# Performance work log

Hardware: AMD Instinct MI355X
Metric: run time of the kernel (lower is better)

The kernel has to match this reference:

```python
import jax, jax.numpy as jnp
import numpy as np
import math

D_MODEL = 1024
NUM_HEADS = 16
B, S = 2, 2048


def setup_inputs() -> dict:
    key = jax.random.key(0)
    ks = jax.random.split(key, 12)
    s = 0.02
    inp = {
        "q": jax.random.normal(ks[0], (B, S, D_MODEL), jnp.float32),
        "k": jax.random.normal(ks[1], (B, S, D_MODEL), jnp.float32),
        "v": jax.random.normal(ks[2], (B, S, D_MODEL), jnp.float32),
        "W_q": jax.random.normal(ks[3], (D_MODEL, D_MODEL), jnp.float32) * s,
        "b_q": jnp.zeros((D_MODEL,), jnp.float32),
        "W_k": jax.random.normal(ks[4], (D_MODEL, D_MODEL), jnp.float32) * s,
        "b_k": jnp.zeros((D_MODEL,), jnp.float32),
        "W_v": jax.random.normal(ks[5], (D_MODEL, D_MODEL), jnp.float32) * s,
        "b_v": jnp.zeros((D_MODEL,), jnp.float32),
        "W_o": jax.random.normal(ks[6], (D_MODEL, D_MODEL), jnp.float32) * s,
        "b_o": jnp.zeros((D_MODEL,), jnp.float32),
        # broadcastable causal mask [1,1,S,S]; masked positions are 0
        "mask": jnp.tril(jnp.ones((S, S), jnp.int32))[None, None, :, :],
    }
    return inp


def reference(q, k, v, W_q, b_q, W_k, b_k, W_v, b_v, W_o, b_o, mask):
    H, d_k = NUM_HEADS, D_MODEL // NUM_HEADS
    Bq, Sq, D = q.shape
    Sk = k.shape[1]
    # Linear projections (torch Linear: x @ W.T + b), split heads -> [B,H,S,d_k]
    qh = (q @ W_q.T + b_q).reshape(Bq, Sq, H, d_k).transpose(0, 2, 1, 3)
    kh = (k @ W_k.T + b_k).reshape(Bq, Sk, H, d_k).transpose(0, 2, 1, 3)
    vh = (v @ W_v.T + b_v).reshape(Bq, Sk, H, d_k).transpose(0, 2, 1, 3)
    # scores [B,H,Sq,Sk]
    scores = jnp.einsum("bhqd,bhkd->bhqk", qh, kh) / math.sqrt(d_k)
    scores = jnp.where(mask == 0, jnp.float32(-jnp.inf), scores)
    attn = jax.nn.softmax(scores, axis=-1)
    context = jnp.einsum("bhqk,bhkd->bhqd", attn, vh)
    context = context.transpose(0, 2, 1, 3).reshape(Bq, Sq, D)
    return context @ W_o.T + b_o
```

## Files before the change

### kernel.cpp

```cpp
#include <hip/hip_runtime.h>
#include <hip/hip_bf16.h>

using f32x4  = __attribute__((ext_vector_type(4))) float;
using f32x16 = __attribute__((ext_vector_type(16))) float;
using short8 = __attribute__((ext_vector_type(8))) short;
using us8    = __attribute__((ext_vector_type(8))) unsigned short;
using us4    = __attribute__((ext_vector_type(4))) unsigned short;
using fl4    = __attribute__((ext_vector_type(4))) float;

__device__ __forceinline__ unsigned short f2bf(float f){
    unsigned u = __builtin_bit_cast(unsigned, f);
    u += 0x7FFF + ((u >> 16) & 1);
    return (unsigned short)(u >> 16);
}

__device__ __forceinline__ unsigned cvtpk_bf16(float lo, float hi){
    unsigned r;
    asm volatile("v_cvt_pk_bf16_f32 %0, %1, %2" : "=v"(r) : "v"(lo), "v"(hi));
    return r;
}

__device__ __forceinline__ void pl32swap(unsigned &a, unsigned &b){
    asm volatile("v_permlane32_swap_b32 %0, %1" : "+v"(a), "+v"(b));
}

__device__ __forceinline__ void gload16(const unsigned short* g, unsigned short* l) {
    __builtin_amdgcn_global_load_lds(
        (const __attribute__((address_space(1))) unsigned int*)g,
        (__attribute__((address_space(3))) unsigned int*)l, 16, 0, 0);
}

__global__ __launch_bounds__(256)
void conv_bf16(const float* __restrict__ s0, const float* __restrict__ s1, const float* __restrict__ s2,
               const float* __restrict__ s3, const float* __restrict__ s4, const float* __restrict__ s5,
               const float* __restrict__ s6,
               unsigned short* __restrict__ d0, unsigned short* __restrict__ d1, unsigned short* __restrict__ d2,
               unsigned short* __restrict__ d3, unsigned short* __restrict__ d4, unsigned short* __restrict__ d5,
               unsigned short* __restrict__ d6,
               int nbig4, int nsml4)
{
    const int z = blockIdx.z;
    const float* s = (z==0)?s0:(z==1)?s1:(z==2)?s2:(z==3)?s3:(z==4)?s4:(z==5)?s5:s6;
    unsigned short* d = (z==0)?d0:(z==1)?d1:(z==2)?d2:(z==3)?d3:(z==4)?d4:(z==5)?d5:d6;
    const int n4 = (z < 3) ? nbig4 : nsml4;
    const int stride = gridDim.x * blockDim.x;
    for (int i = blockIdx.x * blockDim.x + threadIdx.x; i < n4; i += stride) {
        fl4 v = ((const fl4*)s)[i];
        us4 o = { f2bf(v[0]), f2bf(v[1]), f2bf(v[2]), f2bf(v[3]) };
        ((us4*)d)[i] = o;
    }
}

template<bool OBF16>
__global__ __launch_bounds__(256, 2)
void gemm_bf16(const unsigned short* __restrict__ A0, const unsigned short* __restrict__ A1,
               const unsigned short* __restrict__ A2,
               const unsigned short* __restrict__ W0, const unsigned short* __restrict__ W1,
               const unsigned short* __restrict__ W2,
               const float* __restrict__ B0, const float* __restrict__ B1, const float* __restrict__ B2,
               void* __restrict__ O0, void* __restrict__ O1, void* __restrict__ O2,
               int M, int N, int K)
{
    const int z = blockIdx.z;
    const unsigned short* Ap = (z==0)?A0:(z==1)?A1:A2;
    const unsigned short* Wp = (z==0)?W0:(z==1)?W1:W2;
    const float* bp = (z==0)?B0:(z==1)?B1:B2;
    void* Op = (z==0)?O0:(z==1)?O1:O2;

    const int tid = threadIdx.x, lane = tid & 63, w = tid >> 6;
    const int wr = w >> 1, wc = w & 1;
    const int l15 = lane & 15, l4 = lane >> 4;
    const int bm = blockIdx.y, bn = blockIdx.x;

    __shared__ unsigned short As[2][128 * 64];
    __shared__ unsigned short Bs[2][128 * 64];

    f32x4 acc[4][4];
    #pragma unroll
    for (int i = 0; i < 4; i++)
        #pragma unroll
        for (int j = 0; j < 4; j++) acc[i][j] = (f32x4){0.f, 0.f, 0.f, 0.f};

    const int KT = K >> 6;
    const int srow = lane >> 3;
    const int scol = (lane & 7) * 8;

    auto stage = [&](int buf, int kt) {
        #pragma unroll
        for (int i = 0; i < 4; i++) {
            const int chunk = w * 4 + i;
            const int row = chunk * 8 + srow;
            gload16(Ap + (size_t)(bm * 128 + row) * K + kt * 64 + scol, &As[buf][chunk * 512]);
            gload16(Wp + (size_t)(bn * 128 + row) * K + kt * 64 + scol, &Bs[buf][chunk * 512]);
        }
    };

    stage(0, 0);
    int cur = 0;
    for (int kt = 0; kt < KT; ++kt) {
        if (kt + 1 < KT) {
            stage(cur ^ 1, kt + 1);
            asm volatile("s_waitcnt vmcnt(8)" ::: "memory");
        } else {
            asm volatile("s_waitcnt vmcnt(0)" ::: "memory");
        }
        __builtin_amdgcn_s_barrier();

        short8 af[4][2], bfr[4][2];
        #pragma unroll
        for (int mf = 0; mf < 4; mf++)
            #pragma unroll
            for (int kf = 0; kf < 2; kf++)
                af[mf][kf] = *(const short8*)&As[cur][(wr * 64 + mf * 16 + l15) * 64 + kf * 32 + l4 * 8];
        #pragma unroll
        for (int nf = 0; nf < 4; nf++)
            #pragma unroll
            for (int kf = 0; kf < 2; kf++)
                bfr[nf][kf] = *(const short8*)&Bs[cur][(wc * 64 + nf * 16 + l15) * 64 + kf * 32 + l4 * 8];
        #pragma unroll
        for (int mf = 0; mf < 4; mf++)
            #pragma unroll
            for (int nf = 0; nf < 4; nf++)
                #pragma unroll
                for (int kf = 0; kf < 2; kf++)
                    acc[mf][nf] = __builtin_amdgcn_mfma_f32_16x16x32_bf16(af[mf][kf], bfr[nf][kf], acc[mf][nf], 0, 0, 0);

        __builtin_amdgcn_s_barrier();
        cur ^= 1;
    }

    #pragma unroll
    for (int mf = 0; mf < 4; mf++) {
        int row = bm * 128 + wr * 64 + mf * 16 + l4 * 4;
        #pragma unroll
        for (int nf = 0; nf < 4; nf++) {
            int col = bn * 128 + wc * 64 + nf * 16 + l15;
            float bv = bp[col];
            #pragma unroll
            for (int r = 0; r < 4; r++) {
                float vv = acc[mf][nf][r] + bv;
                if constexpr (OBF16)
                    ((unsigned short*)Op)[(size_t)(row + r) * N + col] = f2bf(vv);
                else
                    ((float*)Op)[(size_t)(row + r) * N + col] = vv;
            }
        }
    }
}

__global__ __launch_bounds__(256)
void transpose_v(const unsigned short* __restrict__ Vp, unsigned short* __restrict__ VpT)
{
    const int bh = blockIdx.y, b = bh >> 4, h = bh & 15;
    const int s0 = blockIdx.x * 64;
    const int tid = threadIdx.x;
    __shared__ unsigned short T[64 * 64];
    #pragma unroll
    for (int i = 0; i < 2; i++) {
        int cc = i * 256 + tid, r = cc >> 3, c = cc & 7;
        us8 v = *(const us8*)(Vp + (size_t)(b * 2048 + s0 + r) * 1024 + h * 64 + c * 8);
        int off = (r * 128 + c * 16) ^ ((((r & 7) ^ ((r >> 3) & 7))) << 4);
        *(us8*)((char*)T + off) = v;
    }
    __syncthreads();
    #pragma unroll
    for (int i = 0; i < 2; i++) {
        int cc = i * 256 + tid, d = cc >> 3, c = cc & 7;
        us8 o;
        #pragma unroll
        for (int j = 0; j < 8; j++) {
            int s = c * 8 + j;
            int off = (s * 128 + d * 2) ^ ((((s & 7) ^ ((s >> 3) & 7))) << 4);
            o[j] = *(const unsigned short*)((const char*)T + off);
        }
        *(us8*)(VpT + ((size_t)bh * 64 + d) * 2048 + s0 + c * 8) = o;
    }
}

__global__ __launch_bounds__(128)
void attn_causal(const unsigned short* __restrict__ Qp,
                 const unsigned short* __restrict__ Kp,
                 const unsigned short* __restrict__ VpT,
                 unsigned short* __restrict__ Ctx)
{
    const int S = 2048, D = 1024;
    const int bh = blockIdx.y, b = bh >> 4, h = bh & 15;
    const int pairIdx = blockIdx.x;
    const int tid = threadIdx.x, w = tid >> 6, lane = tid & 63;
    const int l31 = lane & 31, hi = lane >> 5;

    __shared__ unsigned short Ks[64 * 64];
    __shared__ unsigned short Vt[64 * 64];

    const float sc = 0.125f * 1.44269504088896f;

    for (int phase = 0; phase < 2; ++phase) {
        const int qt = (phase == 0) ? pairIdx : 31 - pairIdx;
        const int nt = qt + 1;
        const int qrow = qt * 64 + w * 32 + l31;

        short8 qf[4];
        #pragma unroll
        for (int ks = 0; ks < 4; ks++)
            qf[ks] = *(const short8*)(Qp + (size_t)(b * S + qrow) * D + h * 64 + ks * 16 + hi * 8);

        float mrow = -3.0e38f, lrow = 0.f;
        f32x16 oacc[2];
        #pragma unroll
        for (int dh = 0; dh < 2; dh++)
            #pragma unroll
            for (int r = 0; r < 16; r++) oacc[dh][r] = 0.f;

        us8 krg[4], vtrg[4];
        #pragma unroll
        for (int i = 0; i < 4; i++) {
            int cc = i * 128 + tid, r = cc >> 3, c = cc & 7;
            krg[i]  = *(const us8*)(Kp  + (size_t)(b * S + r) * D + h * 64 + c * 8);
            vtrg[i] = *(const us8*)(VpT + ((size_t)bh * 64 + r) * 2048 + c * 8);
        }

        for (int t = 0; t < nt; ++t) {
            __syncthreads();
            #pragma unroll
            for (int i = 0; i < 4; i++) {
                int cc = i * 128 + tid, r = cc >> 3, c = cc & 7;
                int off = (r * 128 + c * 16) ^ ((r & 7) << 4);
                *(us8*)((char*)Ks + off) = krg[i];
                *(us8*)((char*)Vt + off) = vtrg[i];
            }
            __syncthreads();

            if (t + 1 < nt) {
                #pragma unroll
                for (int i = 0; i < 4; i++) {
                    int cc = i * 128 + tid, r = cc >> 3, c = cc & 7;
                    krg[i]  = *(const us8*)(Kp  + (size_t)(b * S + (t + 1) * 64 + r) * D + h * 64 + c * 8);
                    vtrg[i] = *(const us8*)(VpT + ((size_t)bh * 64 + r) * 2048 + (t + 1) * 64 + c * 8);
                }
            }

            f32x16 sacc[2];
            #pragma unroll
            for (int kvh = 0; kvh < 2; kvh++)
                #pragma unroll
                for (int r = 0; r < 16; r++) sacc[kvh][r] = 0.f;
            #pragma unroll
            for (int kvh = 0; kvh < 2; kvh++)
                #pragma unroll
                for (int ks = 0; ks < 4; ks++) {
                    int row = kvh * 32 + l31;
                    int off = (row * 128 + ks * 32 + hi * 16) ^ ((l31 & 7) << 4);
                    short8 kfrag = *(const short8*)((const char*)Ks + off);
                    sacc[kvh] = __builtin_amdgcn_mfma_f32_32x32x16_bf16(kfrag, qf[ks], sacc[kvh], 0, 0, 0);
                }

            float pf[2][16];
            const bool domask = (t == nt - 1);
            #pragma unroll
            for (int kvh = 0; kvh < 2; kvh++)
                #pragma unroll
                for (int r = 0; r < 16; r++) {
                    float x = sacc[kvh][r] * sc;
                    if (domask) {
                        int kv = t * 64 + kvh * 32 + (r & 3) + 8 * (r >> 2) + 4 * hi;
                        if (kv > qrow) x = -3.0e38f;
                    }
                    pf[kvh][r] = x;
                }

            float pm = -3.0e38f;
            #pragma unroll
            for (int kvh = 0; kvh < 2; kvh++)
                #pragma unroll
                for (int r = 0; r < 16; r++) pm = fmaxf(pm, pf[kvh][r]);
            pm = fmaxf(pm, __shfl_xor(pm, 32));
            float mn = fmaxf(mrow, pm);
            float fs = exp2f(mrow - mn);
            float ps = 0.f;
            #pragma unroll
            for (int kvh = 0; kvh < 2; kvh++)
                #pragma unroll
                for (int r = 0; r < 16; r++) {
                    float e = exp2f(pf[kvh][r] - mn);
                    pf[kvh][r] = e;
                    ps += e;
                }
            ps += __shfl_xor(ps, 32);
            lrow = lrow * fs + ps;
            mrow = mn;
            #pragma unroll
            for (int dh = 0; dh < 2; dh++)
                #pragma unroll
                for (int r = 0; r < 16; r++) oacc[dh][r] *= fs;

            #pragma unroll
            for (int kvh = 0; kvh < 2; kvh++) {
                unsigned w00 = cvtpk_bf16(pf[kvh][0],  pf[kvh][1]);
                unsigned w01 = cvtpk_bf16(pf[kvh][2],  pf[kvh][3]);
                unsigned w10 = cvtpk_bf16(pf[kvh][4],  pf[kvh][5]);
                unsigned w11 = cvtpk_bf16(pf[kvh][6],  pf[kvh][7]);
                unsigned w20 = cvtpk_bf16(pf[kvh][8],  pf[kvh][9]);
                unsigned w21 = cvtpk_bf16(pf[kvh][10], pf[kvh][11]);
                unsigned w30 = cvtpk_bf16(pf[kvh][12], pf[kvh][13]);
                unsigned w31 = cvtpk_bf16(pf[kvh][14], pf[kvh][15]);
                pl32swap(w00, w10);
                pl32swap(w01, w11);
                pl32swap(w20, w30);
                pl32swap(w21, w31);
                unsigned stepA[4] = { w00, w01, w10, w11 };
                unsigned stepB[4] = { w20, w21, w30, w31 };
                short8 bA = __builtin_bit_cast(short8, *(const us8*)stepA);
                short8 bB = __builtin_bit_cast(short8, *(const us8*)stepB);
                #pragma unroll
                for (int dh = 0; dh < 2; dh++) {
                    int row = dh * 32 + l31;
                    int offA = (row * 128 + kvh * 64 + hi * 16) ^ ((l31 & 7) << 4);
                    short8 vA = *(const short8*)((const char*)Vt + offA);
                    oacc[dh] = __builtin_amdgcn_mfma_f32_32x32x16_bf16(vA, bA, oacc[dh], 0, 0, 0);
                    int offB = offA ^ 32;
                    short8 vB = *(const short8*)((const char*)Vt + offB);
                    oacc[dh] = __builtin_amdgcn_mfma_f32_32x32x16_bf16(vB, bB, oacc[dh], 0, 0, 0);
                }
            }
        }

        float invl = 1.0f / lrow;
        #pragma unroll
        for (int dh = 0; dh < 2; dh++)
            #pragma unroll
            for (int tq = 0; tq < 4; tq++) {
                us4 o = { f2bf(oacc[dh][4*tq+0] * invl), f2bf(oacc[dh][4*tq+1] * invl),
                          f2bf(oacc[dh][4*tq+2] * invl), f2bf(oacc[dh][4*tq+3] * invl) };
                int d = dh * 32 + tq * 8 + hi * 4;
                *(us4*)(Ctx + (size_t)(b * S + qrow) * D + h * 64 + d) = o;
            }
    }
}

extern "C" void kernel_launch(void* const* d_in, const int* in_sizes, int n_in,
                              void* d_out, int out_size, void* d_ws, size_t ws_size,
                              hipStream_t stream)
{
    const float* q  = (const float*)d_in[0];
    const float* k  = (const float*)d_in[1];
    const float* v  = (const float*)d_in[2];
    const float* Wq = (const float*)d_in[3];
    const float* bq = (const float*)d_in[4];
    const float* Wk = (const float*)d_in[5];
    const float* bk = (const float*)d_in[6];
    const float* Wv = (const float*)d_in[7];
    const float* bv = (const float*)d_in[8];
    const float* Wo = (const float*)d_in[9];
    const float* bo = (const float*)d_in[10];

    const int M = 4096, N = 1024, K = 1024;
    const size_t nBS = (size_t)M * N;
    const size_t nW  = (size_t)N * K;

    unsigned short* qb   = (unsigned short*)d_ws;
    unsigned short* kb   = qb  + nBS;
    unsigned short* vb   = kb  + nBS;
    unsigned short* Wqb  = vb  + nBS;
    unsigned short* Wkb  = Wqb + nW;
    unsigned short* Wvb  = Wkb + nW;
    unsigned short* Wob  = Wvb + nW;
    unsigned short* Qp   = Wob + nW;
    unsigned short* Kp   = Qp  + nBS;
    unsigned short* Vp   = Kp  + nBS;
    unsigned short* VpT  = Vp  + nBS;
    unsigned short* Ct   = qb;

    dim3 gc(1024, 1, 7);
    conv_bf16<<<gc, 256, 0, stream>>>(q, k, v, Wq, Wk, Wv, Wo,
                                      qb, kb, vb, Wqb, Wkb, Wvb, Wob,
                                      (int)(nBS / 4), (int)(nW / 4));

    dim3 g1(N / 128, M / 128, 3);
    gemm_bf16<true><<<g1, 256, 0, stream>>>(qb, kb, vb, Wqb, Wkb, Wvb,
                                            bq, bk, bv, Qp, Kp, Vp, M, N, K);

    dim3 gt(32, 32);
    transpose_v<<<gt, 256, 0, stream>>>(Vp, VpT);

    dim3 g2(16, 32);
    attn_causal<<<g2, 128, 0, stream>>>(Qp, Kp, VpT, Ct);

    dim3 g3(N / 128, M / 128, 1);
    gemm_bf16<false><<<g3, 256, 0, stream>>>(Ct, Ct, Ct, Wob, Wob, Wob,
                                             bo, bo, bo, d_out, d_out, d_out, M, N, K);
}
```

Baseline: 268.5 us.

## Double-buffer K/V via direct-to-LDS loads, one q-tile per block, lazy softmax rescale

Result: slower. 278.0 us (+3.6%).

```diff
diff --git a/kernel.cpp b/kernel.cpp
--- a/kernel.cpp
+++ b/kernel.cpp
@@ -185,156 +185,163 @@
 {
     const int S = 2048, D = 1024;
     const int bh = blockIdx.y, b = bh >> 4, h = bh & 15;
-    const int pairIdx = blockIdx.x;
+    const int qt = (blockIdx.x + blockIdx.y) & 31;
     const int tid = threadIdx.x, w = tid >> 6, lane = tid & 63;
     const int l31 = lane & 31, hi = lane >> 5;
 
-    __shared__ unsigned short Ks[64 * 64];
-    __shared__ unsigned short Vt[64 * 64];
+    __shared__ unsigned short Ks[2][64 * 64];
+    __shared__ unsigned short Vt[2][64 * 64];
 
     const float sc = 0.125f * 1.44269504088896f;
-
-    for (int phase = 0; phase < 2; ++phase) {
-        const int qt = (phase == 0) ? pairIdx : 31 - pairIdx;
-        const int nt = qt + 1;
-        const int qrow = qt * 64 + w * 32 + l31;
-
-        short8 qf[4];
-        #pragma unroll
-        for (int ks = 0; ks < 4; ks++)
-            qf[ks] = *(const short8*)(Qp + (size_t)(b * S + qrow) * D + h * 64 + ks * 16 + hi * 8);
-
-        float mrow = -3.0e38f, lrow = 0.f;
-        f32x16 oacc[2];
-        #pragma unroll
-        for (int dh = 0; dh < 2; dh++)
-            #pragma unroll
-            for (int r = 0; r < 16; r++) oacc[dh][r] = 0.f;
-
-        us8 krg[4], vtrg[4];
+    const int nt = qt + 1;
+    const int qrow = qt * 64 + w * 32 + l31;
+
+    const int rsub = lane >> 3;
+    const int csw  = (lane & 7) ^ rsub;
+
+    auto stage = [&](int buf, int t) {
         #pragma unroll
         for (int i = 0; i < 4; i++) {
-            int cc = i * 128 + tid, r = cc >> 3, c = cc & 7;
-            krg[i]  = *(const us8*)(Kp  + (size_t)(b * S + r) * D + h * 64 + c * 8);
-            vtrg[i] = *(const us8*)(VpT + ((size_t)bh * 64 + r) * 2048 + c * 8);
-        }
-
-        for (int t = 0; t < nt; ++t) {
-            __syncthreads();
-            #pragma unroll
-            for (int i = 0; i < 4; i++) {
-                int cc = i * 128 + tid, r = cc >> 3, c = cc & 7;
-                int off = (r * 128 + c * 16) ^ ((r & 7) << 4);
-                *(us8*)((char*)Ks + off) = krg[i];
-                *(us8*)((char*)Vt + off) = vtrg[i];
-            }
-            __syncthreads();
-
-            if (t + 1 < nt) {
-                #pragma unroll
-                for (int i = 0; i < 4; i++) {
-                    int cc = i * 128 + tid, r = cc >> 3, c = cc & 7;
-                    krg[i]  = *(const us8*)(Kp  + (size_t)(b * S + (t + 1) * 64 + r) * D + h * 64 + c * 8);
-                    vtrg[i] = *(const us8*)(VpT + ((size_t)bh * 64 + r) * 2048 + (t + 1) * 64 + c * 8);
+            const int r0 = w * 32 + i * 8;
+            gload16(Kp  + (size_t)(b * S + t * 64 + r0 + rsub) * D + h * 64 + csw * 8,
+                    &Ks[buf][r0 * 64]);
+            gload16(VpT + ((size_t)bh * 64 + r0 + rsub) * 2048 + t * 64 + csw * 8,
+                    &Vt[buf][r0 * 64]);
+        }
+    };
+
+    short8 qf[4];
+    #pragma unroll
+    for (int ks = 0; ks < 4; ks++)
+        qf[ks] = *(const short8*)(Qp + (size_t)(b * S + qrow) * D + h * 64 + ks * 16 + hi * 8);
+
+    stage(0, 0);
+    asm volatile("" :: "v"(qf[0]), "v"(qf[1]), "v"(qf[2]), "v"(qf[3]));
+
+    float mrow = -3.0e38f, lrow = 0.f;
+    f32x16 oacc[2];
+    #pragma unroll
+    for (int dh = 0; dh < 2; dh++)
+        #pragma unroll
+        for (int r = 0; r < 16; r++) oacc[dh][r] = 0.f;
+
+    int cur = 0;
+    for (int t = 0; t < nt; ++t) {
+        if (t + 1 < nt) {
+            stage(cur ^ 1, t + 1);
+            asm volatile("s_waitcnt vmcnt(8)" ::: "memory");
+        } else {
+            asm volatile("s_waitcnt vmcnt(0)" ::: "memory");
+        }
+        __builtin_amdgcn_s_barrier();
+        __builtin_amdgcn_sched_barrier(0);
+
+        f32x16 sacc[2];
+        #pragma unroll
+        for (int kvh = 0; kvh < 2; kvh++)
+            #pragma unroll
+            for (int r = 0; r < 16; r++) sacc[kvh][r] = 0.f;
+        #pragma unroll
+        for (int kvh = 0; kvh < 2; kvh++)
+            #pragma unroll
+            for (int ks = 0; ks < 4; ks++) {
+                int row = kvh * 32 + l31;
+                int off = (row * 128 + ks * 32 + hi * 16) ^ ((l31 & 7) << 4);
+                short8 kfrag = *(const short8*)((const char*)Ks[cur] + off);
+                sacc[kvh] = __builtin_amdgcn_mfma_f32_32x32x16_bf16(kfrag, qf[ks], sacc[kvh], 0, 0, 0);
+            }
+
+        float pf[2][16];
+        const bool domask = (t == nt - 1);
+        #pragma unroll
+        for (int kvh = 0; kvh < 2; kvh++)
+            #pragma unroll
+            for (int r = 0; r < 16; r++) {
+                float x = sacc[kvh][r] * sc;
+                if (domask) {
+                    int kv = t * 64 + kvh * 32 + (r & 3) + 8 * (r >> 2) + 4 * hi;
+                    if (kv > qrow) x = -3.0e38f;
                 }
-            }
-
-            f32x16 sacc[2];
-            #pragma unroll
-            for (int kvh = 0; kvh < 2; kvh++)
-                #pragma unroll
-                for (int r = 0; r < 16; r++) sacc[kvh][r] = 0.f;
-            #pragma unroll
-            for (int kvh = 0; kvh < 2; kvh++)
-                #pragma unroll
-                for (int ks = 0; ks < 4; ks++) {
-                    int row = kvh * 32 + l31;
-                    int off = (row * 128 + ks * 32 + hi * 16) ^ ((l31 & 7) << 4);
-                    short8 kfrag = *(const short8*)((const char*)Ks + off);
-                    sacc[kvh] = __builtin_amdgcn_mfma_f32_32x32x16_bf16(kfrag, qf[ks], sacc[kvh], 0, 0, 0);
-                }
-
-            float pf[2][16];
-            const bool domask = (t == nt - 1);
-            #pragma unroll
-            for (int kvh = 0; kvh < 2; kvh++)
-                #pragma unroll
-                for (int r = 0; r < 16; r++) {
-                    float x = sacc[kvh][r] * sc;
-                    if (domask) {
-                        int kv = t * 64 + kvh * 32 + (r & 3) + 8 * (r >> 2) + 4 * hi;
-                        if (kv > qrow) x = -3.0e38f;
-                    }
-                    pf[kvh][r] = x;
-                }
-
-            float pm = -3.0e38f;
-            #pragma unroll
-            for (int kvh = 0; kvh < 2; kvh++)
-                #pragma unroll
-                for (int r = 0; r < 16; r++) pm = fmaxf(pm, pf[kvh][r]);
-            pm = fmaxf(pm, __shfl_xor(pm, 32));
-            float mn = fmaxf(mrow, pm);
+                pf[kvh][r] = x;
+            }
+
+        float pm = -3.0e38f;
+        #pragma unroll
+        for (int kvh = 0; kvh < 2; kvh++)
+            #pragma unroll
+            for (int r = 0; r < 16; r++) pm = fmaxf(pm, pf[kvh][r]);
+        pm = fmaxf(pm, __shfl_xor(pm, 32));
+
+        float mn;
+        if (__all(pm - mrow <= 8.0f)) {
+            mn = mrow;
+        } else {
+            mn = fmaxf(mrow, pm);
             float fs = exp2f(mrow - mn);
-            float ps = 0.f;
-            #pragma unroll
-            for (int kvh = 0; kvh < 2; kvh++)
-                #pragma unroll
-                for (int r = 0; r < 16; r++) {
-                    float e = exp2f(pf[kvh][r] - mn);
-                    pf[kvh][r] = e;
-                    ps += e;
-                }
-            ps += __shfl_xor(ps, 32);
-            lrow = lrow * fs + ps;
-            mrow = mn;
             #pragma unroll
             for (int dh = 0; dh < 2; dh++)
                 #pragma unroll
                 for (int r = 0; r < 16; r++) oacc[dh][r] *= fs;
-
-            #pragma unroll
-            for (int kvh = 0; kvh < 2; kvh++) {
-                unsigned w00 = cvtpk_bf16(pf[kvh][0],  pf[kvh][1]);
-                unsigned w01 = cvtpk_bf16(pf[kvh][2],  pf[kvh][3]);
-                unsigned w10 = cvtpk_bf16(pf[kvh][4],  pf[kvh][5]);
-                unsigned w11 = cvtpk_bf16(pf[kvh][6],  pf[kvh][7]);
-                unsigned w20 = cvtpk_bf16(pf[kvh][8],  pf[kvh][9]);
-                unsigned w21 = cvtpk_bf16(pf[kvh][10], pf[kvh][11]);
-                unsigned w30 = cvtpk_bf16(pf[kvh][12], pf[kvh][13]);
-                unsigned w31 = cvtpk_bf16(pf[kvh][14], pf[kvh][15]);
-                pl32swap(w00, w10);
-                pl32swap(w01, w11);
-                pl32swap(w20, w30);
-                pl32swap(w21, w31);
-                unsigned stepA[4] = { w00, w01, w10, w11 };
-                unsigned stepB[4] = { w20, w21, w30, w31 };
-                short8 bA = __builtin_bit_cast(short8, *(const us8*)stepA);
-                short8 bB = __builtin_bit_cast(short8, *(const us8*)stepB);
-                #pragma unroll
-                for (int dh = 0; dh < 2; dh++) {
-                    int row = dh * 32 + l31;
-                    int offA = (row * 128 + kvh * 64 + hi * 16) ^ ((l31 & 7) << 4);
-                    short8 vA = *(const short8*)((const char*)Vt + offA);
-                    oacc[dh] = __builtin_amdgcn_mfma_f32_32x32x16_bf16(vA, bA, oacc[dh], 0, 0, 0);
-                    int offB = offA ^ 32;
-                    short8 vB = *(const short8*)((const char*)Vt + offB);
-                    oacc[dh] = __builtin_amdgcn_mfma_f32_32x32x16_bf16(vB, bB, oacc[dh], 0, 0, 0);
-                }
-            }
-        }
-
-        float invl = 1.0f / lrow;
-        #pragma unroll
-        for (int dh = 0; dh < 2; dh++)
-            #pragma unroll
-            for (int tq = 0; tq < 4; tq++) {
-                us4 o = { f2bf(oacc[dh][4*tq+0] * invl), f2bf(oacc[dh][4*tq+1] * invl),
-                          f2bf(oacc[dh][4*tq+2] * invl), f2bf(oacc[dh][4*tq+3] * invl) };
-                int d = dh * 32 + tq * 8 + hi * 4;
-                *(us4*)(Ctx + (size_t)(b * S + qrow) * D + h * 64 + d) = o;
-            }
-    }
+            lrow *= fs;
+            mrow = mn;
+        }
+        float ps = 0.f;
+        #pragma unroll
+        for (int kvh = 0; kvh < 2; kvh++)
+            #pragma unroll
+            for (int r = 0; r < 16; r++) {
+                float e = exp2f(pf[kvh][r] - mn);
+                pf[kvh][r] = e;
+                ps += e;
+            }
+        ps += __shfl_xor(ps, 32);
+        lrow += ps;
+
+        #pragma unroll
+        for (int kvh = 0; kvh < 2; kvh++) {
+            unsigned w00 = cvtpk_bf16(pf[kvh][0],  pf[kvh][1]);
+            unsigned w01 = cvtpk_bf16(pf[kvh][2],  pf[kvh][3]);
+            unsigned w10 = cvtpk_bf16(pf[kvh][4],  pf[kvh][5]);
+            unsigned w11 = cvtpk_bf16(pf[kvh][6],  pf[kvh][7]);
+            unsigned w20 = cvtpk_bf16(pf[kvh][8],  pf[kvh][9]);
+            unsigned w21 = cvtpk_bf16(pf[kvh][10], pf[kvh][11]);
+            unsigned w30 = cvtpk_bf16(pf[kvh][12], pf[kvh][13]);
+            unsigned w31 = cvtpk_bf16(pf[kvh][14], pf[kvh][15]);
+            pl32swap(w00, w10);
+            pl32swap(w01, w11);
+            pl32swap(w20, w30);
+            pl32swap(w21, w31);
+            unsigned stepA[4] = { w00, w01, w10, w11 };
+            unsigned stepB[4] = { w20, w21, w30, w31 };
+            short8 bA = __builtin_bit_cast(short8, *(const us8*)stepA);
+            short8 bB = __builtin_bit_cast(short8, *(const us8*)stepB);
+            #pragma unroll
+            for (int dh = 0; dh < 2; dh++) {
+                int row = dh * 32 + l31;
+                int offA = (row * 128 + kvh * 64 + hi * 16) ^ ((l31 & 7) << 4);
+                short8 vA = *(const short8*)((const char*)Vt[cur] + offA);
+                oacc[dh] = __builtin_amdgcn_mfma_f32_32x32x16_bf16(vA, bA, oacc[dh], 0, 0, 0);
+                int offB = offA ^ 32;
+                short8 vB = *(const short8*)((const char*)Vt[cur] + offB);
+                oacc[dh] = __builtin_amdgcn_mfma_f32_32x32x16_bf16(vB, bB, oacc[dh], 0, 0, 0);
+            }
+        }
+
+        __builtin_amdgcn_sched_barrier(0);
+        __builtin_amdgcn_s_barrier();
+        cur ^= 1;
+    }
+
+    float invl = 1.0f / lrow;
+    #pragma unroll
+    for (int dh = 0; dh < 2; dh++)
+        #pragma unroll
+        for (int tq = 0; tq < 4; tq++) {
+            us4 o = { f2bf(oacc[dh][4*tq+0] * invl), f2bf(oacc[dh][4*tq+1] * invl),
+                      f2bf(oacc[dh][4*tq+2] * invl), f2bf(oacc[dh][4*tq+3] * invl) };
+            int d = dh * 32 + tq * 8 + hi * 4;
+            *(us4*)(Ctx + (size_t)(b * S + qrow) * D + h * 64 + d) = o;
+        }
 }
 
 extern "C" void kernel_launch(void* const* d_in, const int* in_sizes, int n_in,
@@ -382,7 +389,7 @@
     dim3 gt(32, 32);
     transpose_v<<<gt, 256, 0, stream>>>(Vp, VpT);
 
-    dim3 g2(16, 32);
+    dim3 g2(32, 32);
     attn_causal<<<g2, 128, 0, stream>>>(Qp, Kp, VpT, Ct);
 
     dim3 g3(N / 128, M / 128, 1);
```
